# Performance work log

Hardware: AMD Instinct MI355X
Metric: run time of the kernel (lower is better)

The kernel has to match this reference:

```python
import jax, jax.numpy as jnp
import numpy as np

N, E, DIN, DH, H = 100000, 500000, 776, 128, 4
C = DH // H          # per-head channels = 32
NEG_SLOPE = 0.2      # PyG GATConv default
LN_EPS = 1e-5        # torch LayerNorm default


def layer_norm(x, g, b):
    mu = x.mean(-1, keepdims=True)
    var = ((x - mu) ** 2).mean(-1, keepdims=True)
    return (x - mu) / jnp.sqrt(var + LN_EPS) * g + b


def gat_conv(x, src, dst, W, att_src, att_dst, bias):
    """PyG GATConv(DH, DH//H, heads=H) with default add_self_loops=True."""
    loops = jnp.arange(N, dtype=src.dtype)
    s = jnp.concatenate([src, loops])  # [E+N]
    d = jnp.concatenate([dst, loops])
    h = (x @ W).reshape(N, H, C)                      # [N,H,C]
    a_s = (h * att_src).sum(-1)                       # [N,H]
    a_d = (h * att_dst).sum(-1)                       # [N,H]
    e = jax.nn.leaky_relu(a_s[s] + a_d[d], NEG_SLOPE)  # [E+N,H]
    m = jax.ops.segment_max(e, d, num_segments=N)     # per-dst max (stable softmax)
    ex = jnp.exp(e - m[d])
    z = jax.ops.segment_sum(ex, d, num_segments=N)
    alpha = ex / z[d]                                 # segment softmax over incoming edges
    out = jax.ops.segment_sum(h[s] * alpha[..., None], d, num_segments=N)  # [N,H,C]
    return out.reshape(N, H * C) + bias


def tgat_layer(x, src, dst, p):
    x_t = layer_norm(x, p['ln_a_g'], p['ln_a_b'])        # TemporalAttention == LayerNorm only
    x_g = gat_conv(x_t, src, dst, p['gat_W'], p['gat_as'], p['gat_ad'], p['gat_b'])
    return layer_norm(x_t + x_g, p['ln_b_g'], p['ln_b_b'])  # dropout is identity (eval)


def setup_inputs() -> dict:
    key = jax.random.key(0)
    ks = jax.random.split(key, 32)
    x = jax.random.normal(ks[0], (N, DIN), dtype=jnp.float32)
    edge_index = jax.random.randint(ks[1], (2, E), 0, N, dtype=jnp.int64)
    timestamps = jax.random.uniform(ks[2], (E,), dtype=jnp.float32)
    sc = 0.05
    d = {
        'x': x, 'edge_index': edge_index, 'timestamps': timestamps,
        'Wp': jax.random.normal(ks[3], (DIN, DH)) * sc,
        'bp': jnp.zeros((DH,)),
        'dp_W1': jax.random.normal(ks[4], (2 * DH, DH)) * sc,
        'dp_b1': jnp.zeros((DH,)),
        'dp_W2': jax.random.normal(ks[5], (DH, 1)) * sc,
        'dp_b2': jnp.zeros((1,)),
    }
    for i in (1, 2):
        k = jax.random.split(ks[5 + i], 4)
        d[f'l{i}_ln_a_g'] = jnp.ones((DH,)); d[f'l{i}_ln_a_b'] = jnp.zeros((DH,))
        d[f'l{i}_gat_W'] = jax.random.normal(k[0], (DH, DH)) * sc
        d[f'l{i}_gat_as'] = jax.random.normal(k[1], (H, C)) * 0.1
        d[f'l{i}_gat_ad'] = jax.random.normal(k[2], (H, C)) * 0.1
        d[f'l{i}_gat_b'] = jnp.zeros((DH,))
        d[f'l{i}_ln_b_g'] = jnp.ones((DH,)); d[f'l{i}_ln_b_b'] = jnp.zeros((DH,))
    return d


def reference(x, edge_index, timestamps, Wp, bp, dp_W1, dp_b1, dp_W2, dp_b2,
              l1_ln_a_g, l1_ln_a_b, l1_gat_W, l1_gat_as, l1_gat_ad, l1_gat_b, l1_ln_b_g, l1_ln_b_b,
              l2_ln_a_g, l2_ln_a_b, l2_gat_W, l2_gat_as, l2_gat_ad, l2_gat_b, l2_ln_b_g, l2_ln_b_b):
    src, dst = edge_index[0], edge_index[1]
    h = x @ Wp + bp  # input projection
    h = tgat_layer(h, src, dst, dict(ln_a_g=l1_ln_a_g, ln_a_b=l1_ln_a_b, gat_W=l1_gat_W,
                                     gat_as=l1_gat_as, gat_ad=l1_gat_ad, gat_b=l1_gat_b,
                                     ln_b_g=l1_ln_b_g, ln_b_b=l1_ln_b_b))
    h = tgat_layer(h, src, dst, dict(ln_a_g=l2_ln_a_g, ln_a_b=l2_ln_a_b, gat_W=l2_gat_W,
                                     gat_as=l2_gat_as, gat_ad=l2_gat_ad, gat_b=l2_gat_b,
                                     ln_b_g=l2_ln_b_g, ln_b_b=l2_ln_b_b))
    # task == 'diffusion': gather src/dst embeddings, cat, 2-layer MLP head -> [E,1]
    ef = jnp.concatenate([h[src], h[dst]], axis=-1)       # [E, 2*DH]
    hid = jax.nn.relu(ef @ dp_W1 + dp_b1)                 # dropout identity (eval)
    return hid @ dp_W2 + dp_b2
```

## Files before the change

kernel.cpp:

```cpp
#include <hip/hip_runtime.h>
#include <math.h>

#define NNODES 100000
#define NEDGES 500000
#define DIN 776
#define DH 128
#define NHEAD 4
#define NEG_SLOPE 0.2f
#define LN_EPS 1e-5f
#define KPAD 832
#define NT_PROJ 13

typedef __attribute__((ext_vector_type(8))) short short8v;
typedef __attribute__((ext_vector_type(4))) float f32x4;

__device__ inline unsigned int f2bf_u(float f) {
    unsigned int u = __float_as_uint(f);
    return (u + 0x7fffu + ((u >> 16) & 1u)) >> 16;
}
__device__ inline float bf2f_lo(unsigned int u) { return __uint_as_float(u << 16); }
__device__ inline float bf2f_hi(unsigned int u) { return __uint_as_float(u & 0xffff0000u); }

#define GLDS16(g, l)                                                      \
    __builtin_amdgcn_global_load_lds(                                     \
        (const __attribute__((address_space(1))) unsigned int*)(g),       \
        (__attribute__((address_space(3))) unsigned int*)(l), 16, 0, 0)

__global__ __launch_bounds__(256) void setup_kernel(const float* __restrict__ Wp,
                                                    const float* __restrict__ gW1,
                                                    const float* __restrict__ gW2,
                                                    const float* __restrict__ W1,
                                                    unsigned short* __restrict__ BtP,
                                                    unsigned short* __restrict__ BtG1,
                                                    unsigned short* __restrict__ BtG2,
                                                    unsigned short* __restrict__ Bt1a,
                                                    unsigned short* __restrict__ Bt1b,
                                                    int* __restrict__ cnt) {
    const int S0 = 128 * KPAD, S = 128 * 128;
    int idx = blockIdx.x * 256 + threadIdx.x;
    if (idx < S0) {
        const int n = idx / KPAD, k = idx % KPAD;
        BtP[idx] = (k < DIN) ? (unsigned short)f2bf_u(Wp[(size_t)k * 128 + n]) : (unsigned short)0;
        return;
    }
    idx -= S0;
    if (idx < S) {
        BtG1[idx] = (unsigned short)f2bf_u(gW1[(size_t)(idx & 127) * 128 + (idx >> 7)]);
        return;
    }
    idx -= S;
    if (idx < S) {
        BtG2[idx] = (unsigned short)f2bf_u(gW2[(size_t)(idx & 127) * 128 + (idx >> 7)]);
        return;
    }
    idx -= S;
    if (idx < S) {
        Bt1a[idx] = (unsigned short)f2bf_u(W1[(size_t)(idx & 127) * 128 + (idx >> 7)]);
        return;
    }
    idx -= S;
    if (idx < S) {
        Bt1b[idx] = (unsigned short)f2bf_u(W1[(size_t)(128 + (idx & 127)) * 128 + (idx >> 7)]);
        return;
    }
    idx -= S;
    if (idx < NNODES) cnt[idx] = 0;
}

__global__ __launch_bounds__(256) void gemm_proj_ln(const float* __restrict__ A,
                                                    const unsigned short* __restrict__ Bt,
                                                    const float* __restrict__ bias,
                                                    const float* __restrict__ lng,
                                                    const float* __restrict__ lnb,
                                                    unsigned short* __restrict__ actb,
                                                    int nrows) {
    constexpr int LSA = 72;
    __shared__ unsigned short As[128 * LSA];
    const int tid = threadIdx.x;
    const int row0 = blockIdx.x * 128;
    const int lane = tid & 63;
    const int wid = tid >> 6;
    const int wr = (wid >> 1) * 64, wc = (wid & 1) * 64;
    const int lrow = lane & 15, hi = lane >> 4, lk = hi * 8;

    int srowv[8], schk[8];
    bool sok[8];
#pragma unroll
    for (int i = 0; i < 8; ++i) {
        const int cid = i * 256 + tid;
        srowv[i] = cid >> 4;
        schk[i] = cid & 15;
        sok[i] = (row0 + srowv[i]) < nrows;
    }

    float4 f[8];
    auto loadA = [&](int t) {
#pragma unroll
        for (int i = 0; i < 8; ++i) {
            const int k = t * 64 + schk[i] * 4;
            f[i] = (sok[i] && (k + 4 <= DIN))
                       ? *(const float4*)(A + (size_t)(row0 + srowv[i]) * DIN + k)
                       : make_float4(0.f, 0.f, 0.f, 0.f);
        }
    };
    auto writeA = [&]() {
#pragma unroll
        for (int i = 0; i < 8; ++i) {
            uint2 q;
            q.x = f2bf_u(f[i].x) | (f2bf_u(f[i].y) << 16);
            q.y = f2bf_u(f[i].z) | (f2bf_u(f[i].w) << 16);
            *(uint2*)&As[srowv[i] * LSA + schk[i] * 4] = q;
        }
    };

    f32x4 acc[4][4];
#pragma unroll
    for (int m = 0; m < 4; ++m)
#pragma unroll
        for (int n = 0; n < 4; ++n) acc[m][n] = (f32x4){0.f, 0.f, 0.f, 0.f};

    loadA(0);
    for (int t = 0; t < NT_PROJ; ++t) {
        writeA();
        __syncthreads();
        if (t + 1 < NT_PROJ) loadA(t + 1);
#pragma unroll
        for (int ks = 0; ks < 2; ++ks) {
            short8v a[4], b[4];
#pragma unroll
            for (int m = 0; m < 4; ++m)
                a[m] = *(const short8v*)&As[(wr + m * 16 + lrow) * LSA + ks * 32 + lk];
#pragma unroll
            for (int n = 0; n < 4; ++n) {
                const int col = wc + n * 16 + lrow;
                b[n] = *(const short8v*)&Bt[(size_t)col * KPAD + t * 64 + ks * 32 + lk];
            }
#pragma unroll
            for (int m = 0; m < 4; ++m)
#pragma unroll
                for (int n = 0; n < 4; ++n)
                    acc[m][n] = __builtin_amdgcn_mfma_f32_16x16x32_bf16(a[m], b[n], acc[m][n], 0, 0, 0);
        }
        __syncthreads();
    }

    float bv[4], gv[4], bb[4];
#pragma unroll
    for (int n = 0; n < 4; ++n) {
        const int col = wc + n * 16 + lrow;
        bv[n] = bias[col];
        gv[n] = lng[col];
        bb[n] = lnb[col];
    }
#pragma unroll
    for (int m = 0; m < 4; ++m)
#pragma unroll
        for (int n = 0; n < 4; ++n)
#pragma unroll
            for (int j = 0; j < 4; ++j) acc[m][n][j] += bv[n];

    float* part = (float*)As;
#pragma unroll
    for (int m = 0; m < 4; ++m) {
#pragma unroll
        for (int j = 0; j < 4; ++j) {
            float s = 0.f, sq = 0.f;
#pragma unroll
            for (int n = 0; n < 4; ++n) {
                const float a = acc[m][n][j];
                s += a;
                sq += a * a;
            }
#pragma unroll
            for (int o = 1; o < 16; o <<= 1) {
                s += __shfl_xor(s, o);
                sq += __shfl_xor(sq, o);
            }
            if (lrow == 0) {
                const int r = wr + m * 16 + hi * 4 + j;
                part[r * 4 + (wid & 1) * 2] = s;
                part[r * 4 + (wid & 1) * 2 + 1] = sq;
            }
        }
    }
    __syncthreads();
#pragma unroll
    for (int m = 0; m < 4; ++m) {
#pragma unroll
        for (int j = 0; j < 4; ++j) {
            const int rloc = wr + m * 16 + hi * 4 + j;
            const int rg = row0 + rloc;
            const float4 p = *(const float4*)&part[rloc * 4];
            const float s = p.x + p.z, sq = p.y + p.w;
            const float mu = s * (1.f / 128.f);
            const float rinv = rsqrtf(sq * (1.f / 128.f) - mu * mu + LN_EPS);
            if (rg < nrows) {
#pragma unroll
                for (int n = 0; n < 4; ++n) {
                    const int col = wc + n * 16 + lrow;
                    const float o = (acc[m][n][j] - mu) * rinv * gv[n] + bb[n];
                    actb[(size_t)rg * 128 + col] = (unsigned short)f2bf_u(o);
                }
            }
        }
    }
}

template<bool ASAD>
__global__ __launch_bounds__(256) void gemm_k128(const unsigned short* __restrict__ Ab,
                                                 const unsigned short* __restrict__ Bt,
                                                 const float* __restrict__ bias,
                                                 const float* __restrict__ gas,
                                                 const float* __restrict__ gad,
                                                 unsigned short* __restrict__ Cb,
                                                 float* __restrict__ a_s,
                                                 float* __restrict__ a_d, int nrows) {
    __shared__ unsigned short As[128 * 128];
    const int tid = threadIdx.x, lane = tid & 63, wid = tid >> 6;
    const int row0 = blockIdx.x * 128;
    const int lrow = lane & 15, hi = lane >> 4, lk = hi * 8;
    const int wr = (wid >> 1) * 64, wc = (wid & 1) * 64;

    {
        const int l4 = lane >> 4, le = lane & 15;
#pragma unroll
        for (int i = 0; i < 8; ++i) {
            const int row = wid * 32 + i * 4 + l4;
            const int kk = (le ^ ((i * 4 + l4) & 7)) << 3;
            const unsigned short* g = Ab + (size_t)(row0 + row) * 128 + kk;
            GLDS16(g, &As[wid * 4096 + i * 512]);
        }
    }
    __syncthreads();

    f32x4 acc[4][4];
#pragma unroll
    for (int m = 0; m < 4; ++m)
#pragma unroll
        for (int n = 0; n < 4; ++n) acc[m][n] = (f32x4){0.f, 0.f, 0.f, 0.f};

#pragma unroll
    for (int ks = 0; ks < 4; ++ks) {
        short8v a[4];
#pragma unroll
        for (int m = 0; m < 4; ++m) {
            const int row = wr + m * 16 + lrow;
            const int e = (ks * 32 + lk) ^ ((row & 7) << 3);
            a[m] = *(const short8v*)&As[row * 128 + e];
        }
#pragma unroll
        for (int n = 0; n < 4; ++n) {
            const int col = wc + n * 16 + lrow;
            const short8v b = *(const short8v*)&Bt[(size_t)col * 128 + ks * 32 + lk];
#pragma unroll
            for (int m = 0; m < 4; ++m)
                acc[m][n] = __builtin_amdgcn_mfma_f32_16x16x32_bf16(a[m], b, acc[m][n], 0, 0, 0);
        }
    }

    const bool hasBias = (bias != nullptr);
#pragma unroll
    for (int m = 0; m < 4; ++m) {
        const int rbase = row0 + wr + m * 16 + hi * 4;
#pragma unroll
        for (int j = 0; j < 4; ++j) {
            const int r = rbase + j;
            if (r < nrows) {
#pragma unroll
                for (int n = 0; n < 4; ++n) {
                    const int col = wc + n * 16 + lrow;
                    const float bv = hasBias ? bias[col] : 0.f;
                    Cb[(size_t)r * 128 + col] = (unsigned short)f2bf_u(acc[m][n][j] + bv);
                }
            }
        }
    }

    if (ASAD) {
        const int h0 = (wid & 1) * 2;
        float vs[4], vd[4];
#pragma unroll
        for (int n = 0; n < 4; ++n) {
            const int ai = (h0 + (n >> 1)) * 32 + (n & 1) * 16 + lrow;
            vs[n] = gas[ai];
            vd[n] = gad[ai];
        }
#pragma unroll
        for (int m = 0; m < 4; ++m) {
#pragma unroll
            for (int j = 0; j < 4; ++j) {
                float ps0 = acc[m][0][j] * vs[0] + acc[m][1][j] * vs[1];
                float ps1 = acc[m][2][j] * vs[2] + acc[m][3][j] * vs[3];
                float pd0 = acc[m][0][j] * vd[0] + acc[m][1][j] * vd[1];
                float pd1 = acc[m][2][j] * vd[2] + acc[m][3][j] * vd[3];
#pragma unroll
                for (int o = 1; o < 16; o <<= 1) {
                    ps0 += __shfl_xor(ps0, o);
                    ps1 += __shfl_xor(ps1, o);
                    pd0 += __shfl_xor(pd0, o);
                    pd1 += __shfl_xor(pd1, o);
                }
                if (lrow == 0) {
                    const int r = row0 + wr + m * 16 + hi * 4 + j;
                    if (r < nrows) {
                        a_s[(size_t)r * 4 + h0] = ps0;
                        a_s[(size_t)r * 4 + h0 + 1] = ps1;
                        a_d[(size_t)r * 4 + h0] = pd0;
                        a_d[(size_t)r * 4 + h0 + 1] = pd1;
                    }
                }
            }
        }
    }
}

__global__ __launch_bounds__(256) void csr_hist(const int* __restrict__ dst,
                                                int* __restrict__ cnt, int ne, int n) {
    const int e = blockIdx.x * 256 + threadIdx.x;
    if (e >= ne + n) return;
    const int d = (e < ne) ? dst[e] : (e - ne);
    atomicAdd(&cnt[d], 1);
}

__global__ __launch_bounds__(256) void csr_scan1(const int* __restrict__ cnt,
                                                 int* __restrict__ offs,
                                                 int* __restrict__ bsum, int n) {
    __shared__ int lds[256];
    const int i = blockIdx.x * 256 + threadIdx.x;
    int v = (i < n) ? cnt[i] : 0;
    lds[threadIdx.x] = v;
    __syncthreads();
    int acc = v;
#pragma unroll
    for (int o = 1; o < 256; o <<= 1) {
        int t = (threadIdx.x >= o) ? lds[threadIdx.x - o] : 0;
        __syncthreads();
        acc += t;
        lds[threadIdx.x] = acc;
        __syncthreads();
    }
    if (i < n) offs[i] = acc - v;
    if (threadIdx.x == 255) bsum[blockIdx.x] = acc;
}

__global__ __launch_bounds__(512) void csr_scan2(int* __restrict__ bsum, int nb) {
    __shared__ int lds[512];
    const int t = threadIdx.x;
    int v = (t < nb) ? bsum[t] : 0;
    lds[t] = v;
    __syncthreads();
    int acc = v;
#pragma unroll
    for (int o = 1; o < 512; o <<= 1) {
        int x = (t >= o) ? lds[t - o] : 0;
        __syncthreads();
        acc += x;
        lds[t] = acc;
        __syncthreads();
    }
    if (t < nb) bsum[t] = acc - v;
}

__global__ __launch_bounds__(256) void csr_scan3(int* __restrict__ offs,
                                                 const int* __restrict__ bsum,
                                                 int* __restrict__ cur, int n, int total) {
    const int i = blockIdx.x * 256 + threadIdx.x;
    if (i < n) {
        const int o = offs[i] + bsum[blockIdx.x];
        offs[i] = o;
        cur[i] = o;
    }
    if (i == 0) offs[n] = total;
}

__global__ __launch_bounds__(256) void csr_scatter(const int* __restrict__ src,
                                                   const int* __restrict__ dst,
                                                   int* __restrict__ cur,
                                                   int* __restrict__ csr, int ne, int n) {
    const int e = blockIdx.x * 256 + threadIdx.x;
    if (e >= ne + n) return;
    int s, d;
    if (e < ne) { s = src[e]; d = dst[e]; } else { s = d = e - ne; }
    const int slot = atomicAdd(&cur[d], 1);
    csr[slot] = s;
}

template<int MODE>
__global__ __launch_bounds__(256) void aggr_ln_kernel(const int* __restrict__ csr,
                                                      const int* __restrict__ offs,
                                                      const float* __restrict__ a_s,
                                                      const float* __restrict__ a_d,
                                                      const unsigned short* __restrict__ hWb,
                                                      const float* __restrict__ gbias,
                                                      const float* __restrict__ g1,
                                                      const float* __restrict__ b1,
                                                      const float* __restrict__ g2,
                                                      const float* __restrict__ b2,
                                                      unsigned short* __restrict__ actb, int n) {
    const int d = (blockIdx.x * blockDim.x + threadIdx.x) >> 6;
    const int lane = threadIdx.x & 63;
    if (d >= n) return;
    const int h = lane >> 4;
    const int beg = offs[d], end = offs[d + 1];
    const float ad = a_d[(size_t)d * 4 + h];

    float z = 0.f, ax = 0.f, ay = 0.f;
    for (int c = beg; c < end; c += 64) {
        const int nj = min(64, end - c);
        const int idx = (c + lane < end) ? csr[c + lane] : 0;
        int j = 0;
        for (; j + 3 < nj; j += 4) {
            const int s0 = __shfl(idx, j);
            const int s1 = __shfl(idx, j + 1);
            const int s2 = __shfl(idx, j + 2);
            const int s3 = __shfl(idx, j + 3);
            const float as0 = a_s[(size_t)s0 * 4 + h];
            const float as1 = a_s[(size_t)s1 * 4 + h];
            const float as2 = a_s[(size_t)s2 * 4 + h];
            const float as3 = a_s[(size_t)s3 * 4 + h];
            const unsigned int u0 = reinterpret_cast<const unsigned int*>(hWb + (size_t)s0 * 128)[lane];
            const unsigned int u1 = reinterpret_cast<const unsigned int*>(hWb + (size_t)s1 * 128)[lane];
            const unsigned int u2 = reinterpret_cast<const unsigned int*>(hWb + (size_t)s2 * 128)[lane];
            const unsigned int u3 = reinterpret_cast<const unsigned int*>(hWb + (size_t)s3 * 128)[lane];
            float x0 = as0 + ad; x0 = x0 > 0.f ? x0 : NEG_SLOPE * x0;
            float x1 = as1 + ad; x1 = x1 > 0.f ? x1 : NEG_SLOPE * x1;
            float x2 = as2 + ad; x2 = x2 > 0.f ? x2 : NEG_SLOPE * x2;
            float x3 = as3 + ad; x3 = x3 > 0.f ? x3 : NEG_SLOPE * x3;
            const float p0 = __expf(x0), p1 = __expf(x1);
            const float p2 = __expf(x2), p3 = __expf(x3);
            z += (p0 + p1) + (p2 + p3);
            ax += p0 * bf2f_lo(u0) + p1 * bf2f_lo(u1) + p2 * bf2f_lo(u2) + p3 * bf2f_lo(u3);
            ay += p0 * bf2f_hi(u0) + p1 * bf2f_hi(u1) + p2 * bf2f_hi(u2) + p3 * bf2f_hi(u3);
        }
        for (; j < nj; ++j) {
            const int s0 = __shfl(idx, j);
            float x0 = a_s[(size_t)s0 * 4 + h] + ad;
            x0 = x0 > 0.f ? x0 : NEG_SLOPE * x0;
            const float p0 = __expf(x0);
            const unsigned int u0 = reinterpret_cast<const unsigned int*>(hWb + (size_t)s0 * 128)[lane];
            z += p0;
            ax += p0 * bf2f_lo(u0);
            ay += p0 * bf2f_hi(u0);
        }
    }
    const float rz = 1.f / z;

    const unsigned int tu = reinterpret_cast<const unsigned int*>(actb + (size_t)d * 128)[lane];
    const float2 gb = reinterpret_cast<const float2*>(gbias)[lane];
    float2 v;
    v.x = bf2f_lo(tu) + ax * rz + gb.x;
    v.y = bf2f_hi(tu) + ay * rz + gb.y;
    float s = v.x + v.y, sq = v.x * v.x + v.y * v.y;
#pragma unroll
    for (int o = 32; o; o >>= 1) { s += __shfl_xor(s, o); sq += __shfl_xor(sq, o); }
    float mu = s * (1.f / 128.f);
    float rinv = rsqrtf(sq * (1.f / 128.f) - mu * mu + LN_EPS);
    const float2 gg1 = reinterpret_cast<const float2*>(g1)[lane];
    const float2 bb1 = reinterpret_cast<const float2*>(b1)[lane];
    float2 y;
    y.x = (v.x - mu) * rinv * gg1.x + bb1.x;
    y.y = (v.y - mu) * rinv * gg1.y + bb1.y;
    if (MODE == 0) {
        s = y.x + y.y; sq = y.x * y.x + y.y * y.y;
#pragma unroll
        for (int o = 32; o; o >>= 1) { s += __shfl_xor(s, o); sq += __shfl_xor(sq, o); }
        mu = s * (1.f / 128.f);
        rinv = rsqrtf(sq * (1.f / 128.f) - mu * mu + LN_EPS);
        const float2 gg2 = reinterpret_cast<const float2*>(g2)[lane];
        const float2 bb2 = reinterpret_cast<const float2*>(b2)[lane];
        float2 o2;
        o2.x = (y.x - mu) * rinv * gg2.x + bb2.x;
        o2.y = (y.y - mu) * rinv * gg2.y + bb2.y;
        reinterpret_cast<unsigned int*>(actb + (size_t)d * 128)[lane] =
            f2bf_u(o2.x) | (f2bf_u(o2.y) << 16);
    } else {
        reinterpret_cast<unsigned int*>(actb + (size_t)d * 128)[lane] =
            f2bf_u(y.x) | (f2bf_u(y.y) << 16);
    }
}

__global__ __launch_bounds__(256) void head_kernel(const int* __restrict__ src,
                                                   const int* __restrict__ dst,
                                                   const unsigned short* __restrict__ Asb,
                                                   const unsigned short* __restrict__ Adb,
                                                   const float* __restrict__ W2,
                                                   const float* __restrict__ b2,
                                                   float* __restrict__ out, int ne) {
    const int wave = (blockIdx.x * blockDim.x + threadIdx.x) >> 6;
    const int lane = threadIdx.x & 63;
    const int e0 = wave * 64;
    if (e0 >= ne) return;
    const int nj = min(64, ne - e0);
    const bool valid = (e0 + lane) < ne;
    const int sidx = valid ? src[e0 + lane] : 0;
    const int didx = valid ? dst[e0 + lane] : 0;
    const float2 w = reinterpret_cast<const float2*>(W2)[lane];
    const float bb = b2[0];
    float outv = 0.f;
    for (int j = 0; j < nj; ++j) {
        const int s = __shfl(sidx, j);
        const int d = __shfl(didx, j);
        const unsigned int ua =
            reinterpret_cast<const unsigned int*>(Asb + (size_t)s * 128)[lane];
        const unsigned int ub =
            reinterpret_cast<const unsigned int*>(Adb + (size_t)d * 128)[lane];
        float h0 = bf2f_lo(ua) + bf2f_lo(ub); h0 = fmaxf(h0, 0.f);
        float h1 = bf2f_hi(ua) + bf2f_hi(ub); h1 = fmaxf(h1, 0.f);
        float t = h0 * w.x + h1 * w.y;
#pragma unroll
        for (int o = 32; o; o >>= 1) t += __shfl_xor(t, o);
        if (lane == j) outv = t + bb;
    }
    if (valid) out[e0 + lane] = outv;
}

extern "C" void kernel_launch(void* const* d_in, const int* in_sizes, int n_in,
                              void* d_out, int out_size, void* d_ws, size_t ws_size,
                              hipStream_t stream) {
    const int N = NNODES, E = NEDGES;
    const float* x  = (const float*)d_in[0];
    const int* ei   = (const int*)d_in[1];
    const int* src  = ei;
    const int* dst  = ei + E;
    const float* Wp = (const float*)d_in[3];
    const float* bp = (const float*)d_in[4];
    const float* W1 = (const float*)d_in[5];
    const float* b1 = (const float*)d_in[6];
    const float* W2 = (const float*)d_in[7];
    const float* b2 = (const float*)d_in[8];
    const float* l1_ln_a_g = (const float*)d_in[9];
    const float* l1_ln_a_b = (const float*)d_in[10];
    const float* gW1  = (const float*)d_in[11];
    const float* gas1 = (const float*)d_in[12];
    const float* gad1 = (const float*)d_in[13];
    const float* gb1  = (const float*)d_in[14];
    const float* l1_ln_b_g = (const float*)d_in[15];
    const float* l1_ln_b_b = (const float*)d_in[16];
    const float* l2_ln_a_g = (const float*)d_in[17];
    const float* l2_ln_a_b = (const float*)d_in[18];
    const float* gW2  = (const float*)d_in[19];
    const float* gas2 = (const float*)d_in[20];
    const float* gad2 = (const float*)d_in[21];
    const float* gb2  = (const float*)d_in[22];
    const float* l2_ln_b_g = (const float*)d_in[23];
    const float* l2_ln_b_b = (const float*)d_in[24];

    float* ws = (float*)d_ws;
    float* a_s  = ws;
    float* a_d  = a_s + (size_t)N * 4;
    unsigned short* actb = (unsigned short*)(a_d + (size_t)N * 4);
    unsigned short* hWb  = actb + (size_t)N * 128;
    unsigned short* Asb  = hWb + (size_t)N * 128;
    unsigned short* Adb  = Asb + (size_t)N * 128;
    unsigned short* BtP  = Adb + (size_t)N * 128;
    unsigned short* BtG1 = BtP + 128 * KPAD;
    unsigned short* BtG2 = BtG1 + 128 * 128;
    unsigned short* Bt1a = BtG2 + 128 * 128;
    unsigned short* Bt1b = Bt1a + 128 * 128;
    int* cnt  = (int*)(Bt1b + 128 * 128);
    int* offs = cnt + N;
    int* bsum = offs + N + 1;
    int* csr  = bsum + 512;

    const int gemmGrid = (N + 127) / 128;
    const int edgeTot = E + N;
    const int edgeGrid = (edgeTot + 255) / 256;
    const int scanBlocks = (N + 255) / 256;
    const int aggrGrid = (N * 64 + 255) / 256;
    const int headWaves = (E + 63) / 64;
    const int headGrid = (headWaves + 3) / 4;
    const int setupTot = 128 * KPAD + 4 * 128 * 128 + N;

    setup_kernel<<<(setupTot + 255) / 256, 256, 0, stream>>>(Wp, gW1, gW2, W1, BtP, BtG1,
                                                             BtG2, Bt1a, Bt1b, cnt);
    csr_hist<<<edgeGrid, 256, 0, stream>>>(dst, cnt, E, N);
    csr_scan1<<<scanBlocks, 256, 0, stream>>>(cnt, offs, bsum, N);
    csr_scan2<<<1, 512, 0, stream>>>(bsum, scanBlocks);
    csr_scan3<<<scanBlocks, 256, 0, stream>>>(offs, bsum, cnt, N, edgeTot);
    csr_scatter<<<edgeGrid, 256, 0, stream>>>(src, dst, cnt, csr, E, N);

    gemm_proj_ln<<<gemmGrid, 256, 0, stream>>>(x, BtP, bp, l1_ln_a_g, l1_ln_a_b, actb, N);

    gemm_k128<true><<<gemmGrid, 256, 0, stream>>>(actb, BtG1, nullptr, gas1, gad1,
                                                  hWb, a_s, a_d, N);
    aggr_ln_kernel<0><<<aggrGrid, 256, 0, stream>>>(csr, offs, a_s, a_d, hWb, gb1,
                                                    l1_ln_b_g, l1_ln_b_b, l2_ln_a_g,
                                                    l2_ln_a_b, actb, N);
    gemm_k128<true><<<gemmGrid, 256, 0, stream>>>(actb, BtG2, nullptr, gas2, gad2,
                                                  hWb, a_s, a_d, N);
    aggr_ln_kernel<1><<<aggrGrid, 256, 0, stream>>>(csr, offs, a_s, a_d, hWb, gb2,
                                                    l2_ln_b_g, l2_ln_b_b, nullptr,
                                                    nullptr, actb, N);

    gemm_k128<false><<<gemmGrid, 256, 0, stream>>>(actb, Bt1a, b1, nullptr, nullptr,
                                                   Asb, nullptr, nullptr, N);
    gemm_k128<false><<<gemmGrid, 256, 0, stream>>>(actb, Bt1b, nullptr, nullptr, nullptr,
                                                   Adb, nullptr, nullptr, N);
    head_kernel<<<headGrid, 256, 0, stream>>>(src, dst, Asb, Adb, W2, b2,
                                              (float*)d_out, E);
}
```

Measured before the change: 480.2 us.

## Double-buffer A prefetch in projection GEMM and merge head GEMMs into one launch

```diff
diff --git a/kernel.cpp b/kernel.cpp
--- a/kernel.cpp
+++ b/kernel.cpp
@@ -67,13 +67,13 @@
     if (idx < NNODES) cnt[idx] = 0;
 }
 
-__global__ __launch_bounds__(256) void gemm_proj_ln(const float* __restrict__ A,
-                                                    const unsigned short* __restrict__ Bt,
-                                                    const float* __restrict__ bias,
-                                                    const float* __restrict__ lng,
-                                                    const float* __restrict__ lnb,
-                                                    unsigned short* __restrict__ actb,
-                                                    int nrows) {
+__global__ __launch_bounds__(256, 3) void gemm_proj_ln(const float* __restrict__ A,
+                                                       const unsigned short* __restrict__ Bt,
+                                                       const float* __restrict__ bias,
+                                                       const float* __restrict__ lng,
+                                                       const float* __restrict__ lnb,
+                                                       unsigned short* __restrict__ actb,
+                                                       int nrows) {
     constexpr int LSA = 72;
     __shared__ unsigned short As[128 * LSA];
     const int tid = threadIdx.x;
@@ -93,8 +93,8 @@
         sok[i] = (row0 + srowv[i]) < nrows;
     }
 
-    float4 f[8];
-    auto loadA = [&](int t) {
+    float4 fA[8], fB[8];
+    auto loadA = [&](float4* f, int t) {
 #pragma unroll
         for (int i = 0; i < 8; ++i) {
             const int k = t * 64 + schk[i] * 4;
@@ -103,7 +103,7 @@
                        : make_float4(0.f, 0.f, 0.f, 0.f);
         }
     };
-    auto writeA = [&]() {
+    auto writeA = [&](const float4* f) {
 #pragma unroll
         for (int i = 0; i < 8; ++i) {
             uint2 q;
@@ -119,11 +119,7 @@
 #pragma unroll
         for (int n = 0; n < 4; ++n) acc[m][n] = (f32x4){0.f, 0.f, 0.f, 0.f};
 
-    loadA(0);
-    for (int t = 0; t < NT_PROJ; ++t) {
-        writeA();
-        __syncthreads();
-        if (t + 1 < NT_PROJ) loadA(t + 1);
+    auto mfma_tile = [&](int t) {
 #pragma unroll
         for (int ks = 0; ks < 2; ++ks) {
             short8v a[4], b[4];
@@ -141,7 +137,25 @@
                 for (int n = 0; n < 4; ++n)
                     acc[m][n] = __builtin_amdgcn_mfma_f32_16x16x32_bf16(a[m], b[n], acc[m][n], 0, 0, 0);
         }
+    };
+
+    loadA(fA, 0);
+    loadA(fB, 1);
+#pragma unroll
+    for (int tp = 0; tp < 7; ++tp) {
+        const int t0 = 2 * tp;
+        writeA(fA);
         __syncthreads();
+        if (t0 + 2 < NT_PROJ) loadA(fA, t0 + 2);
+        mfma_tile(t0);
+        __syncthreads();
+        if (t0 + 1 < NT_PROJ) {
+            writeA(fB);
+            __syncthreads();
+            if (t0 + 3 < NT_PROJ) loadA(fB, t0 + 3);
+            mfma_tile(t0 + 1);
+            __syncthreads();
+        }
     }
 
     float bv[4], gv[4], bb[4];
@@ -308,6 +322,81 @@
                         a_d[(size_t)r * 4 + h0] = pd0;
                         a_d[(size_t)r * 4 + h0 + 1] = pd1;
                     }
+                }
+            }
+        }
+    }
+}
+
+__global__ __launch_bounds__(256) void gemm_k128_head(const unsigned short* __restrict__ Ab,
+                                                      const unsigned short* __restrict__ Bt1,
+                                                      const unsigned short* __restrict__ Bt2,
+                                                      const float* __restrict__ bias1,
+                                                      unsigned short* __restrict__ C1,
+                                                      unsigned short* __restrict__ C2,
+                                                      int nrows, int gridHalf) {
+    const bool second = (int)blockIdx.x >= gridHalf;
+    const unsigned short* Bt = second ? Bt2 : Bt1;
+    unsigned short* Cb = second ? C2 : C1;
+    const float* bias = second ? nullptr : bias1;
+    const int bid = second ? (blockIdx.x - gridHalf) : blockIdx.x;
+
+    __shared__ unsigned short As[128 * 128];
+    const int tid = threadIdx.x, lane = tid & 63, wid = tid >> 6;
+    const int row0 = bid * 128;
+    const int lrow = lane & 15, hi = lane >> 4, lk = hi * 8;
+    const int wr = (wid >> 1) * 64, wc = (wid & 1) * 64;
+
+    {
+        const int l4 = lane >> 4, le = lane & 15;
+#pragma unroll
+        for (int i = 0; i < 8; ++i) {
+            const int row = wid * 32 + i * 4 + l4;
+            const int kk = (le ^ ((i * 4 + l4) & 7)) << 3;
+            const unsigned short* g = Ab + (size_t)(row0 + row) * 128 + kk;
+            GLDS16(g, &As[wid * 4096 + i * 512]);
+        }
+    }
+    __syncthreads();
+
+    f32x4 acc[4][4];
+#pragma unroll
+    for (int m = 0; m < 4; ++m)
+#pragma unroll
+        for (int n = 0; n < 4; ++n) acc[m][n] = (f32x4){0.f, 0.f, 0.f, 0.f};
+
+#pragma unroll
+    for (int ks = 0; ks < 4; ++ks) {
+        short8v a[4];
+#pragma unroll
+        for (int m = 0; m < 4; ++m) {
+            const int row = wr + m * 16 + lrow;
+            const int e = (ks * 32 + lk) ^ ((row & 7) << 3);
+            a[m] = *(const short8v*)&As[row * 128 + e];
+        }
+#pragma unroll
+        for (int n = 0; n < 4; ++n) {
+            const int col = wc + n * 16 + lrow;
+            const short8v b = *(const short8v*)&Bt[(size_t)col * 128 + ks * 32 + lk];
+#pragma unroll
+            for (int m = 0; m < 4; ++m)
+                acc[m][n] = __builtin_amdgcn_mfma_f32_16x16x32_bf16(a[m], b, acc[m][n], 0, 0, 0);
+        }
+    }
+
+    const bool hasBias = (bias != nullptr);
+#pragma unroll
+    for (int m = 0; m < 4; ++m) {
+        const int rbase = row0 + wr + m * 16 + hi * 4;
+#pragma unroll
+        for (int j = 0; j < 4; ++j) {
+            const int r = rbase + j;
+            if (r < nrows) {
+#pragma unroll
+                for (int n = 0; n < 4; ++n) {
+                    const int col = wc + n * 16 + lrow;
+                    const float bv = hasBias ? bias[col] : 0.f;
+                    Cb[(size_t)r * 128 + col] = (unsigned short)f2bf_u(acc[m][n][j] + bv);
                 }
             }
         }
@@ -592,10 +681,8 @@
                                                     l2_ln_b_g, l2_ln_b_b, nullptr,
                                                     nullptr, actb, N);
 
-    gemm_k128<false><<<gemmGrid, 256, 0, stream>>>(actb, Bt1a, b1, nullptr, nullptr,
-                                                   Asb, nullptr, nullptr, N);
-    gemm_k128<false><<<gemmGrid, 256, 0, stream>>>(actb, Bt1b, nullptr, nullptr, nullptr,
-                                                   Adb, nullptr, nullptr, N);
+    gemm_k128_head<<<2 * gemmGrid, 256, 0, stream>>>(actb, Bt1a, Bt1b, b1, Asb, Adb,
+                                                     N, gemmGrid);
     head_kernel<<<headGrid, 256, 0, stream>>>(src, dst, Asb, Adb, W2, b2,
                                               (float*)d_out, E);
 }
```

After: 621.6 us. 29.4% more time.
